# Optimization experiments

Measured on AMD Instinct MI355X. Metric: run time of the kernel, lower is better.

The kernel has to match this reference:

```python
import jax, jax.numpy as jnp
import numpy as np

DIM = 512
HEADS = 8
WIN = 64


def setup_inputs() -> dict:
    key = jax.random.key(0)
    k1, k2, k3 = jax.random.split(key, 3)
    x = jax.random.normal(k1, (16, 4096, DIM), dtype=jnp.float32)
    Wqkv = jax.random.normal(k2, (DIM, 3 * DIM), dtype=jnp.float32) * 0.02
    Wproj = jax.random.normal(k3, (DIM, DIM), dtype=jnp.float32) * 0.02
    bproj = jnp.zeros((DIM,), dtype=jnp.float32)
    return {"x": x, "Wqkv": Wqkv, "Wproj": Wproj, "bproj": bproj}


def reference(x, Wqkv, Wproj, bproj):
    B0, T0, C = x.shape
    H = HEADS
    hd = C // H
    scale = hd ** -0.5
    # reshape sequence into fixed-size windows: [Bw, W, C]
    xw = x.reshape(-1, WIN, C)
    Bw = xw.shape[0]
    # fused QKV projection (no bias)
    qkv = (xw @ Wqkv).reshape(Bw, WIN, 3, H, hd)
    qkv = jnp.transpose(qkv, (2, 0, 3, 1, 4))  # [3, Bw, H, W, hd]
    q, k, v = qkv[0], qkv[1], qkv[2]
    attn = jnp.einsum('bhqd,bhkd->bhqk', q, k) * scale  # [Bw, H, W, W]
    # causal mask within each window
    mask = jnp.tril(jnp.ones((WIN, WIN), dtype=bool))
    attn = jnp.where(mask, attn, -jnp.inf)
    attn = jax.nn.softmax(attn, axis=-1)
    # faithful to source: second (unconditional) softmax applied on probabilities
    attn = jax.nn.softmax(attn, axis=-1)
    out = jnp.einsum('bhqk,bhkd->bhqd', attn, v)  # [Bw, H, W, hd]
    out = jnp.transpose(out, (0, 2, 1, 3)).reshape(Bw, WIN, C)
    out = out @ Wproj + bproj
    return out.reshape(B0, T0, C)
```

## Files before the change

### kernel.cpp

```cpp
#include <hip/hip_runtime.h>


typedef _Float16 f16x8 __attribute__((ext_vector_type(8)));
typedef _Float16 f16x4 __attribute__((ext_vector_type(4)));
typedef float f32x4 __attribute__((ext_vector_type(4)));

#define MFMA16(a, b, c) __builtin_amdgcn_mfma_f32_16x16x32_f16((a), (b), (c), 0, 0, 0)

__device__ __forceinline__ int swz64(int r, int c) { return r * 64 + (c ^ ((r & 7) << 3)); }
__device__ __forceinline__ int swz512(int r, int c) { return r * 512 + (c ^ ((r & 7) << 3)); }

typedef const __attribute__((address_space(1))) void* gas1_t;
typedef __attribute__((address_space(3))) void* las3_t;

__device__ __forceinline__ void stage16(const _Float16* g, _Float16* lbase, int lane) {
#if __has_builtin(__builtin_amdgcn_global_load_lds)
  __builtin_amdgcn_global_load_lds((gas1_t)(const void*)g, (las3_t)(void*)lbase, 16, 0, 0);
#else
  *(f16x8*)(lbase + lane * 8) = *(const f16x8*)g;
#endif
}

__global__ void prep_weights(const float* __restrict__ Wqkv,
                             const float* __restrict__ Wproj,
                             _Float16* __restrict__ wqkvP,
                             _Float16* __restrict__ wprojP) {
  int idx = blockIdx.x * blockDim.x + threadIdx.x;
  if (idx < 786432) {
    int r16 = idx >> 13;
    int rem = idx & 8191;
    int kt = rem >> 9;
    int lane = (rem >> 3) & 63;
    int e = rem & 7;
    int row = r16 * 16 + (lane & 15);
    int k = kt * 32 + (lane >> 4) * 8 + e;
    float v = Wqkv[k * 1536 + row];
    if (row < 512) v *= 0.125f;
    wqkvP[idx] = (_Float16)v;
  } else {
    int j = idx - 786432;
    int r16 = j >> 13;
    int rem = j & 8191;
    int kt = rem >> 9;
    int lane = (rem >> 3) & 63;
    int e = rem & 7;
    int n = r16 * 16 + (lane & 15);
    int k = kt * 32 + (lane >> 4) * 8 + e;
    wprojP[j] = (_Float16)Wproj[k * 512 + n];
  }
}

__global__ __launch_bounds__(512) void prep_x(const float* __restrict__ x,
                                              _Float16* __restrict__ xP) {
  __shared__ __align__(16) _Float16 sX[64 * 512];
  const int tid = threadIdx.x;
  const float4* xv = (const float4*)(x + (size_t)blockIdx.x * 32768);
#pragma unroll
  for (int it = 0; it < 8; ++it) {
    int g = tid + it * 512;
    int r = g >> 6, c0 = (g & 63) << 3;
    float4 a = xv[(r << 7) + (c0 >> 2)];
    float4 b = xv[(r << 7) + (c0 >> 2) + 1];
    f16x8 hv;
    hv[0] = (_Float16)a.x; hv[1] = (_Float16)a.y;
    hv[2] = (_Float16)a.z; hv[3] = (_Float16)a.w;
    hv[4] = (_Float16)b.x; hv[5] = (_Float16)b.y;
    hv[6] = (_Float16)b.z; hv[7] = (_Float16)b.w;
    *(f16x8*)&sX[swz512(r, c0)] = hv;
  }
  __syncthreads();
  _Float16* dst = xP + (size_t)blockIdx.x * 32768;
#pragma unroll
  for (int it = 0; it < 8; ++it) {
    int c8 = tid + it * 512;
    int rt = c8 >> 10, ks = (c8 >> 6) & 15, ln = c8 & 63;
    int row = rt * 16 + (ln & 15);
    int k0 = ks * 32 + (ln >> 4) * 8;
    f16x8 v = *(const f16x8*)&sX[swz512(row, k0)];
    *(f16x8*)(dst + c8 * 8) = v;
  }
}

template <int MODE>
__global__ __launch_bounds__(1024, 4) void gemmT(
    const _Float16* __restrict__ Afp, const _Float16* __restrict__ Bfp,
    _Float16* __restrict__ dst16, float* __restrict__ out,
    const float* __restrict__ bproj) {
  __shared__ __align__(16) _Float16 sG[2][2][16][512];
  const int tid = threadIdx.x;
  const int wid = tid >> 6;
  const int lane = tid & 63;
  const int lg = lane >> 4, lr = lane & 15;
  const int wr = wid >> 2, wc = wid & 3;
  const int r0 = blockIdx.x * 256, c0 = blockIdx.y * 256;

  const _Float16* aS = Afp + (size_t)((r0 >> 4) + wid) * 8192 + lane * 8;
  const _Float16* bS = Bfp + (size_t)((c0 >> 4) + wid) * 8192 + lane * 8;

  const f32x4 zero4 = {0.f, 0.f, 0.f, 0.f};
  f32x4 acc[4][4];
#pragma unroll
  for (int i = 0; i < 4; ++i)
#pragma unroll
    for (int j = 0; j < 4; ++j) acc[i][j] = zero4;

  stage16(aS, &sG[0][0][wid][0], lane);
  stage16(bS, &sG[0][1][wid][0], lane);
  __syncthreads();

  for (int kt = 0; kt < 16; ++kt) {
    const int cur = kt & 1;
    if (kt < 15) {
      stage16(aS + (kt + 1) * 512, &sG[cur ^ 1][0][wid][0], lane);
      stage16(bS + (kt + 1) * 512, &sG[cur ^ 1][1][wid][0], lane);
    }
    f16x8 af[4], bf[4];
#pragma unroll
    for (int mi = 0; mi < 4; ++mi)
      af[mi] = *(const f16x8*)&sG[cur][0][wr * 4 + mi][lane * 8];
#pragma unroll
    for (int ni = 0; ni < 4; ++ni)
      bf[ni] = *(const f16x8*)&sG[cur][1][wc * 4 + ni][lane * 8];
#pragma unroll
    for (int mi = 0; mi < 4; ++mi)
#pragma unroll
      for (int ni = 0; ni < 4; ++ni)
        acc[mi][ni] = MFMA16(af[mi], bf[ni], acc[mi][ni]);
    __syncthreads();
  }

  if constexpr (MODE == 0) {
#pragma unroll
    for (int mi = 0; mi < 4; ++mi) {
      int nb = r0 + wr * 64 + mi * 16 + lg * 4;
      int sec = nb >> 9, h = (nb >> 6) & 7, db = nb & 63;
      int e0 = db & 7;
      int coff = (db >> 5) * 512 + (((db >> 3) & 3) * 16) * 8 + e0;
#pragma unroll
      for (int ni = 0; ni < 4; ++ni) {
        int tg = c0 + wc * 64 + ni * 16 + lr;
        int w = tg >> 6, t = tg & 63;
        size_t pos = ((size_t)w * 24 + sec * 8 + h) * 4096 +
                     (size_t)((t >> 4) * 2) * 512 + coff + (t & 15) * 8;
        f16x4 hv;
        hv[0] = (_Float16)acc[mi][ni][0]; hv[1] = (_Float16)acc[mi][ni][1];
        hv[2] = (_Float16)acc[mi][ni][2]; hv[3] = (_Float16)acc[mi][ni][3];
        *(f16x4*)(dst16 + pos) = hv;
      }
    }
  } else if constexpr (MODE == 1) {
#pragma unroll
    for (int mi = 0; mi < 4; ++mi) {
      int tbg = r0 + wr * 64 + mi * 16 + lg * 4;
      int w = tbg >> 6, tb = tbg & 63;
      int e0 = tb & 7;
      int coff = (tb >> 5) * 512 + (((tb >> 3) & 3) * 16) * 8 + e0;
#pragma unroll
      for (int ni = 0; ni < 4; ++ni) {
        int cv = c0 + wc * 64 + ni * 16 + lr;
        int h = cv >> 6, d = cv & 63;
        size_t pos = ((size_t)w * 24 + 16 + h) * 4096 +
                     (size_t)((d >> 4) * 2) * 512 + coff + (d & 15) * 8;
        f16x4 hv;
        hv[0] = (_Float16)acc[mi][ni][0]; hv[1] = (_Float16)acc[mi][ni][1];
        hv[2] = (_Float16)acc[mi][ni][2]; hv[3] = (_Float16)acc[mi][ni][3];
        *(f16x4*)(dst16 + pos) = hv;
      }
    }
  } else {
#pragma unroll
    for (int mi = 0; mi < 4; ++mi) {
      int nb = r0 + wr * 64 + mi * 16 + lg * 4;
      float4 bi = *(const float4*)&bproj[nb];
#pragma unroll
      for (int ni = 0; ni < 4; ++ni) {
        int tg = c0 + wc * 64 + ni * 16 + lr;
        float4 v;
        v.x = acc[mi][ni][0] + bi.x; v.y = acc[mi][ni][1] + bi.y;
        v.z = acc[mi][ni][2] + bi.z; v.w = acc[mi][ni][3] + bi.w;
        *(float4*)&out[(size_t)tg * 512 + nb] = v;
      }
    }
  }
}

__global__ __launch_bounds__(512, 4) void attn_win(
    const _Float16* __restrict__ qkvP, _Float16* __restrict__ hP) {
  __shared__ __align__(16) _Float16 sP[4][4096];
  const int tid = threadIdx.x;
  const int wid = tid >> 6;
  const int lane = tid & 63;
  const int lg = lane >> 4, lr = lane & 15;
  const int hl = wid >> 1, part = wid & 1;
  const int w = blockIdx.x;
  const f32x4 zero4 = {0.f, 0.f, 0.f, 0.f};

  for (int hr = 0; hr < 2; ++hr) {
    const int h = hr * 4 + hl;
    const _Float16* Qb = qkvP + ((size_t)w * 24 + h) * 4096 + lane * 8;
    const _Float16* Kb = qkvP + ((size_t)w * 24 + 8 + h) * 4096 + lane * 8;
    const _Float16* Vb = qkvP + ((size_t)w * 24 + 16 + h) * 4096 + lane * 8;

    f16x8 afq[2][2], bfk[4][2];
#pragma unroll
    for (int rs = 0; rs < 2; ++rs)
#pragma unroll
      for (int dkt = 0; dkt < 2; ++dkt)
        afq[rs][dkt] = *(const f16x8*)(Qb + ((part * 2 + rs) * 2 + dkt) * 512);
#pragma unroll
    for (int nt = 0; nt < 4; ++nt)
#pragma unroll
      for (int dkt = 0; dkt < 2; ++dkt)
        bfk[nt][dkt] = *(const f16x8*)(Kb + (nt * 2 + dkt) * 512);
    f32x4 sacc[2][4];
#pragma unroll
    for (int rs = 0; rs < 2; ++rs)
#pragma unroll
      for (int nt = 0; nt < 4; ++nt) sacc[rs][nt] = zero4;
#pragma unroll
    for (int dkt = 0; dkt < 2; ++dkt)
#pragma unroll
      for (int rs = 0; rs < 2; ++rs)
#pragma unroll
        for (int nt = 0; nt < 4; ++nt)
          sacc[rs][nt] = MFMA16(afq[rs][dkt], bfk[nt][dkt], sacc[rs][nt]);

    f16x8 afv[2][2];
#pragma unroll
    for (int ds = 0; ds < 2; ++ds)
#pragma unroll
      for (int tkt = 0; tkt < 2; ++tkt)
        afv[ds][tkt] = *(const f16x8*)(Vb + ((part * 2 + ds) * 2 + tkt) * 512);

    float p2[2][4][4];
#pragma unroll
    for (int rs = 0; rs < 2; ++rs) {
      const int rsg = part * 2 + rs;
#pragma unroll
      for (int rg = 0; rg < 4; ++rg) {
        int row = rsg * 16 + lg * 4 + rg;
        float m = -1e30f;
#pragma unroll
        for (int nt = 0; nt < 4; ++nt) {
          int col = nt * 16 + lr;
          float v = (col <= row) ? sacc[rs][nt][rg] : -1e30f;
          m = fmaxf(m, v);
        }
#pragma unroll
        for (int off = 8; off >= 1; off >>= 1) m = fmaxf(m, __shfl_xor(m, off));
        float e[4], s1 = 0.f;
#pragma unroll
        for (int nt = 0; nt < 4; ++nt) {
          int col = nt * 16 + lr;
          e[nt] = (col <= row) ? __expf(sacc[rs][nt][rg] - m) : 0.f;
          s1 += e[nt];
        }
#pragma unroll
        for (int off = 8; off >= 1; off >>= 1) s1 += __shfl_xor(s1, off);
        float inv1 = 1.f / s1;
        float e2[4], s2 = 0.f;
#pragma unroll
        for (int nt = 0; nt < 4; ++nt) {
          e2[nt] = __expf(e[nt] * inv1);
          s2 += e2[nt];
        }
#pragma unroll
        for (int off = 8; off >= 1; off >>= 1) s2 += __shfl_xor(s2, off);
        float inv2 = 1.f / s2;
#pragma unroll
        for (int nt = 0; nt < 4; ++nt) p2[rs][nt][rg] = e2[nt] * inv2;
      }
    }

#pragma unroll
    for (int rs = 0; rs < 2; ++rs) {
      const int rsg = part * 2 + rs;
#pragma unroll
      for (int nt = 0; nt < 4; ++nt) {
        int cbase = (rsg * 2 + (nt >> 1)) * 512 +
                    ((((nt * 2) + (lr >> 3)) & 3) * 16 + lg * 4) * 8 + (lr & 7);
#pragma unroll
        for (int rg = 0; rg < 4; ++rg)
          sP[hl][cbase + rg * 8] = (_Float16)p2[rs][nt][rg];
      }
    }
    __syncthreads();

    f32x4 oacc[2][4];
#pragma unroll
    for (int ds = 0; ds < 2; ++ds)
#pragma unroll
      for (int ntq = 0; ntq < 4; ++ntq) oacc[ds][ntq] = zero4;
#pragma unroll
    for (int tkt = 0; tkt < 2; ++tkt) {
      f16x8 bfp[4];
#pragma unroll
      for (int ntq = 0; ntq < 4; ++ntq)
        bfp[ntq] = *(const f16x8*)&sP[hl][(ntq * 2 + tkt) * 512 + lane * 8];
#pragma unroll
      for (int ds = 0; ds < 2; ++ds)
#pragma unroll
        for (int ntq = 0; ntq < 4; ++ntq)
          oacc[ds][ntq] = MFMA16(afv[ds][tkt], bfp[ntq], oacc[ds][ntq]);
    }

#pragma unroll
    for (int ds = 0; ds < 2; ++ds) {
      const int dsg = part * 2 + ds;
      const int e0 = (lg & 1) * 4;
      const int lgt = (dsg * 2 + (lg >> 1)) & 3;
#pragma unroll
      for (int ntq = 0; ntq < 4; ++ntq) {
        size_t pos = ((size_t)(w * 4 + ntq) * 16 + h * 2 + (dsg >> 1)) * 512 +
                     (lgt * 16 + lr) * 8 + e0;
        f16x4 hv;
        hv[0] = (_Float16)oacc[ds][ntq][0]; hv[1] = (_Float16)oacc[ds][ntq][1];
        hv[2] = (_Float16)oacc[ds][ntq][2]; hv[3] = (_Float16)oacc[ds][ntq][3];
        *(f16x4*)(hP + pos) = hv;
      }
    }
    __syncthreads();
  }
}

__global__ __launch_bounds__(512, 2) void attn_fused(
    const float* __restrict__ x, const _Float16* __restrict__ wqkvP,
    const _Float16* __restrict__ wprojP, const float* __restrict__ bproj,
    float* __restrict__ out) {
  __shared__ __align__(16) _Float16 sX[64 * 512];
  __shared__ __align__(16) _Float16 sHeads[4][2][4096];

  const int tid = threadIdx.x;
  const int wid = tid >> 6;
  const int lane = tid & 63;
  const int lg = lane >> 4;
  const int lr = lane & 15;

  _Float16* sQ0 = &sHeads[0][0][0];
  _Float16* sK0 = &sHeads[1][0][0];
  _Float16* sVT0 = &sHeads[2][0][0];
  _Float16* sPO0 = &sHeads[3][0][0];

  const float4* xv = (const float4*)(x + (size_t)blockIdx.x * 32768);
#pragma unroll
  for (int it = 0; it < 8; ++it) {
    int g = tid + it * 512;
    int r = g >> 6, c0 = (g & 63) << 3;
    float4 a = xv[(r << 7) + (c0 >> 2)];
    float4 b = xv[(r << 7) + (c0 >> 2) + 1];
    f16x8 hv;
    hv[0] = (_Float16)a.x; hv[1] = (_Float16)a.y;
    hv[2] = (_Float16)a.z; hv[3] = (_Float16)a.w;
    hv[4] = (_Float16)b.x; hv[5] = (_Float16)b.y;
    hv[6] = (_Float16)b.z; hv[7] = (_Float16)b.w;
    *(f16x8*)&sX[swz512(r, c0)] = hv;
  }
  const f32x4 zero4 = {0.f, 0.f, 0.f, 0.f};
  f32x4 accO[4][4];
#pragma unroll
  for (int i = 0; i < 4; ++i)
#pragma unroll
    for (int j = 0; j < 4; ++j) accO[i][j] = zero4;
  __syncthreads();

  for (int hp = 0; hp < 4; ++hp) {
    int hu[3], su[3], stu[3];
    const _Float16* bp[3];
    f32x4 acc[3][4];
#pragma unroll
    for (int i = 0; i < 3; ++i) {
      int u = wid + 8 * i;
      int hh = u & 1, v2 = u >> 1;
      int sec = v2 % 3, strip = v2 / 3;
      hu[i] = hh; su[i] = sec; stu[i] = strip;
      int r16 = sec * 32 + (hp * 2 + hh) * 4 + strip;
      bp[i] = wqkvP + (size_t)r16 * 8192 + lane * 8;
#pragma unroll
      for (int rt = 0; rt < 4; ++rt) acc[i][rt] = zero4;
    }
    f16x8 bf[3][3];
#pragma unroll
    for (int d = 0; d < 3; ++d)
#pragma unroll
      for (int i = 0; i < 3; ++i) bf[d][i] = *(const f16x8*)(bp[i] + d * 512);
    f16x8 af[2][4];
#pragma unroll
    for (int rt = 0; rt < 4; ++rt)
      af[0][rt] = *(const f16x8*)&sX[swz512(rt * 16 + lr, lg * 8)];
#pragma unroll
    for (int ks = 0; ks < 16; ++ks) {
      if (ks < 15) {
#pragma unroll
        for (int rt = 0; rt < 4; ++rt)
          af[(ks + 1) & 1][rt] =
              *(const f16x8*)&sX[swz512(rt * 16 + lr, (ks + 1) * 32 + lg * 8)];
      }
#pragma unroll
      for (int i = 0; i < 3; ++i)
#pragma unroll
        for (int rt = 0; rt < 4; ++rt)
          acc[i][rt] = MFMA16(af[ks & 1][rt], bf[ks % 3][i], acc[i][rt]);
      if (ks + 3 < 16) {
#pragma unroll
        for (int i = 0; i < 3; ++i)
          bf[ks % 3][i] = *(const f16x8*)(bp[i] + (ks + 3) * 512);
      }
    }
#pragma unroll
    for (int i = 0; i < 3; ++i) {
      int hh = hu[i], sec = su[i], strip = stu[i];
      _Float16* dq = sQ0 + hh * 4096;
      _Float16* dk = sK0 + hh * 4096;
      _Float16* dv = sVT0 + hh * 4096;
#pragma unroll
      for (int rt = 0; rt < 4; ++rt)
#pragma unroll
        for (int rg = 0; rg < 4; ++rg) {
          int row = rt * 16 + lg * 4 + rg;
          int col = strip * 16 + lr;
          _Float16 v = (_Float16)acc[i][rt][rg];
          if (sec == 0) dq[swz64(row, col)] = v;
          else if (sec == 1) dk[swz64(row, col)] = v;
          else dv[swz64(col, row)] = v;
        }
    }
    __syncthreads();
    {
      const int hh = wid >> 2;
      const int rs = wid & 3;
      const _Float16* mQ = sQ0 + hh * 4096;
      const _Float16* mK = sK0 + hh * 4096;
      const _Float16* mV = sVT0 + hh * 4096;
      _Float16* mP = sPO0 + hh * 4096;
      f32x4 sacc[4];
#pragma unroll
      for (int nt = 0; nt < 4; ++nt) sacc[nt] = zero4;
#pragma unroll
      for (int ks = 0; ks < 2; ++ks) {
        f16x8 afq = *(const f16x8*)&mQ[swz64(rs * 16 + lr, ks * 32 + lg * 8)];
#pragma unroll
        for (int nt = 0; nt < 4; ++nt) {
          f16x8 bfk = *(const f16x8*)&mK[swz64(nt * 16 + lr, ks * 32 + lg * 8)];
          sacc[nt] = MFMA16(afq, bfk, sacc[nt]);
        }
      }
      float p2[4][4];
#pragma unroll
      for (int rg = 0; rg < 4; ++rg) {
        int row = rs * 16 + lg * 4 + rg;
        float m = -1e30f;
#pragma unroll
        for (int nt = 0; nt < 4; ++nt) {
          int col = nt * 16 + lr;
          float v = (col <= row) ? sacc[nt][rg] : -1e30f;
          m = fmaxf(m, v);
        }
#pragma unroll
        for (int off = 8; off >= 1; off >>= 1) m = fmaxf(m, __shfl_xor(m, off));
        float e[4], s1 = 0.f;
#pragma unroll
        for (int nt = 0; nt < 4; ++nt) {
          int col = nt * 16 + lr;
          e[nt] = (col <= row) ? __expf(sacc[nt][rg] - m) : 0.f;
          s1 += e[nt];
        }
#pragma unroll
        for (int off = 8; off >= 1; off >>= 1) s1 += __shfl_xor(s1, off);
        float inv1 = 1.f / s1;
        float e2[4], s2 = 0.f;
#pragma unroll
        for (int nt = 0; nt < 4; ++nt) {
          e2[nt] = __expf(e[nt] * inv1);
          s2 += e2[nt];
        }
#pragma unroll
        for (int off = 8; off >= 1; off >>= 1) s2 += __shfl_xor(s2, off);
        float inv2 = 1.f / s2;
#pragma unroll
        for (int nt = 0; nt < 4; ++nt) p2[nt][rg] = e2[nt] * inv2;
      }
#pragma unroll
      for (int nt = 0; nt < 4; ++nt)
#pragma unroll
        for (int rg = 0; rg < 4; ++rg)
          mP[swz64(rs * 16 + lg * 4 + rg, nt * 16 + lr)] = (_Float16)p2[nt][rg];
      asm volatile("" ::: "memory");
      f32x4 oacc[4];
#pragma unroll
      for (int nt = 0; nt < 4; ++nt) oacc[nt] = zero4;
#pragma unroll
      for (int ks = 0; ks < 2; ++ks) {
        f16x8 afp = *(const f16x8*)&mP[swz64(rs * 16 + lr, ks * 32 + lg * 8)];
#pragma unroll
        for (int nt = 0; nt < 4; ++nt) {
          f16x8 bfv = *(const f16x8*)&mV[swz64(nt * 16 + lr, ks * 32 + lg * 8)];
          oacc[nt] = MFMA16(afp, bfv, oacc[nt]);
        }
      }
      asm volatile("" ::: "memory");
#pragma unroll
      for (int nt = 0; nt < 4; ++nt)
#pragma unroll
        for (int rg = 0; rg < 4; ++rg)
          mP[swz64(rs * 16 + lg * 4 + rg, nt * 16 + lr)] = (_Float16)oacc[nt][rg];
    }
    __syncthreads();
    {
      f16x8 bfC[2][4], afC[2][4];
#pragma unroll
      for (int rt = 0; rt < 4; ++rt)
        afC[0][rt] = *(const f16x8*)&sPO0[swz64(rt * 16 + lr, lg * 8)];
#pragma unroll
      for (int nt = 0; nt < 4; ++nt)
        bfC[0][nt] = *(const f16x8*)(wprojP + (size_t)(wid * 4 + nt) * 8192 +
                                     (size_t)(hp * 4) * 512 + lane * 8);
#pragma unroll
      for (int g = 0; g < 4; ++g) {
        if (g < 3) {
          int hn = (g + 1) >> 1, kn = (g + 1) & 1;
#pragma unroll
          for (int rt = 0; rt < 4; ++rt)
            afC[(g + 1) & 1][rt] = *(const f16x8*)&sPO0[hn * 4096 +
                swz64(rt * 16 + lr, kn * 32 + lg * 8)];
#pragma unroll
          for (int nt = 0; nt < 4; ++nt)
            bfC[(g + 1) & 1][nt] =
                *(const f16x8*)(wprojP + (size_t)(wid * 4 + nt) * 8192 +
                                (size_t)(hp * 4 + g + 1) * 512 + lane * 8);
        }
#pragma unroll
        for (int nt = 0; nt < 4; ++nt)
#pragma unroll
          for (int rt = 0; rt < 4; ++rt)
            accO[rt][nt] = MFMA16(afC[g & 1][rt], bfC[g & 1][nt], accO[rt][nt]);
      }
    }
  }
  __syncthreads();
  float bias_r[4];
#pragma unroll
  for (int nt = 0; nt < 4; ++nt) bias_r[nt] = bproj[wid * 64 + nt * 16 + lr];
  float* sEp = (float*)&sHeads[0][0][0];
  size_t base = (size_t)blockIdx.x * 32768;
#pragma unroll
  for (int half = 0; half < 2; ++half) {
#pragma unroll
    for (int rr = 0; rr < 2; ++rr) {
      int rt = half * 2 + rr;
#pragma unroll
      for (int nt = 0; nt < 4; ++nt)
#pragma unroll
        for (int rg = 0; rg < 4; ++rg) {
          int r = rr * 16 + lg * 4 + rg;
          int c = wid * 64 + nt * 16 + lr;
          sEp[r * 512 + (c ^ (((r >> 2) & 1) << 4))] = accO[rt][nt][rg] + bias_r[nt];
        }
    }
    __syncthreads();
#pragma unroll
    for (int j = 0; j < 8; ++j) {
      int f4 = tid + j * 512;
      int r = f4 >> 7;
      int c0 = (f4 & 127) << 2;
      float4 v = *(const float4*)&sEp[r * 512 + (c0 ^ (((r >> 2) & 1) << 4))];
      *(float4*)&out[base + (size_t)(half * 32 + r) * 512 + c0] = v;
    }
    if (half == 0) __syncthreads();
  }
}

extern "C" void kernel_launch(void* const* d_in, const int* in_sizes, int n_in,
                              void* d_out, int out_size, void* d_ws, size_t ws_size,
                              hipStream_t stream) {
  const float* x = (const float*)d_in[0];
  const float* Wqkv = (const float*)d_in[1];
  const float* Wproj = (const float*)d_in[2];
  const float* bproj = (const float*)d_in[3];
  float* out = (float*)d_out;

  const size_t W1 = 786432, W2 = 262144, XN = 33554432;
  const size_t QN = 100663296, HN = 33554432;
  _Float16* wqkvP = (_Float16*)d_ws;
  _Float16* wprojP = wqkvP + W1;
  _Float16* xP = wprojP + W2;
  _Float16* qkvP = xP + XN;
  _Float16* hP = qkvP + QN;
  const size_t NEED = (W1 + W2 + XN + QN + HN) * 2;

  prep_weights<<<dim3(4096), dim3(256), 0, stream>>>(Wqkv, Wproj, wqkvP, wprojP);
  if (ws_size >= NEED) {
    prep_x<<<dim3(1024), dim3(512), 0, stream>>>(x, xP);
    gemmT<0><<<dim3(4, 256), dim3(1024), 0, stream>>>(wqkvP, xP, qkvP, nullptr, nullptr);
    gemmT<1><<<dim3(256, 2), dim3(1024), 0, stream>>>(xP, wqkvP + (size_t)64 * 8192,
                                                      qkvP, nullptr, nullptr);
    attn_win<<<dim3(1024), dim3(512), 0, stream>>>(qkvP, hP);
    gemmT<2><<<dim3(2, 256), dim3(1024), 0, stream>>>(wprojP, hP, nullptr, out, bproj);
  } else {
    attn_fused<<<dim3(1024), dim3(512), 0, stream>>>(x, wqkvP, wprojP, bproj, out);
  }
}
```

Baseline: 312.8 us.

## Replace GEMM kernels with 8-wave ping-pong pipelined GEMM and XCD-aware tile swizzle

Replaces the 16-wave 256x256 GEMM with an 8-wave version in which each wave computes a 128x64 sub-tile. K is processed in 64-wide steps, and loading the next stage is interleaved with four quarter-MFMA phases separated by raw s_barrier and explicit vmcnt waits. MFMA sections run at raised s_setprio. The block index is remapped round-robin across 8 groups so neighbouring tiles share L2. The intent is to hide global-to-LDS latency behind MFMA work and raise MFMA density per wave, at the cost of more registers (launch bounds 512,2), many barriers, and hand-written waitcnt logic that is fragile to get right.

```diff
diff --git a/kernel.cpp b/kernel.cpp
--- a/kernel.cpp
+++ b/kernel.cpp
@@ -20,6 +20,9 @@
   *(f16x8*)(lbase + lane * 8) = *(const f16x8*)g;
 #endif
 }
+
+#define CFENCE() asm volatile("" ::: "memory")
+#define BARRIER() do { CFENCE(); __builtin_amdgcn_s_barrier(); CFENCE(); } while (0)
 
 __global__ void prep_weights(const float* __restrict__ Wqkv,
                              const float* __restrict__ Wproj,
@@ -81,61 +84,141 @@
   }
 }
 
+__device__ __forceinline__ void ds_a4(const _Float16* base, int chunkBase, int lane8,
+                                      f16x8 (&a)[4][2]) {
+#pragma unroll
+  for (int mi = 0; mi < 4; ++mi)
+#pragma unroll
+    for (int kt = 0; kt < 2; ++kt)
+      a[mi][kt] = *(const f16x8*)(base + (chunkBase + mi * 2 + kt) * 512 + lane8);
+}
+
+__device__ __forceinline__ void ds_b2(const _Float16* base, int chunkBase, int lane8,
+                                      f16x8 (&b)[2][2]) {
+#pragma unroll
+  for (int ni = 0; ni < 2; ++ni)
+#pragma unroll
+    for (int kt = 0; kt < 2; ++kt)
+      b[ni][kt] = *(const f16x8*)(base + (chunkBase + ni * 2 + kt) * 512 + lane8);
+}
+
+__device__ __forceinline__ void mma_q(const f16x8 (&a)[4][2], const f16x8 (&b)[2][2],
+                                      f32x4 (&acc)[8][4], int rh, int ch) {
+  __builtin_amdgcn_s_setprio(1);
+#pragma unroll
+  for (int kt = 0; kt < 2; ++kt)
+#pragma unroll
+    for (int mi = 0; mi < 4; ++mi)
+#pragma unroll
+      for (int ni = 0; ni < 2; ++ni)
+        acc[rh * 4 + mi][ch * 2 + ni] =
+            MFMA16(a[mi][kt], b[ni][kt], acc[rh * 4 + mi][ch * 2 + ni]);
+  __builtin_amdgcn_s_setprio(0);
+}
+
 template <int MODE>
-__global__ __launch_bounds__(1024, 4) void gemmT(
+__global__ __launch_bounds__(512, 2) void gemm8(
     const _Float16* __restrict__ Afp, const _Float16* __restrict__ Bfp,
     _Float16* __restrict__ dst16, float* __restrict__ out,
-    const float* __restrict__ bproj) {
-  __shared__ __align__(16) _Float16 sG[2][2][16][512];
+    const float* __restrict__ bproj, int rTiles) {
+  __shared__ __align__(16) _Float16 sG[2][2][32][512];
   const int tid = threadIdx.x;
   const int wid = tid >> 6;
   const int lane = tid & 63;
   const int lg = lane >> 4, lr = lane & 15;
   const int wr = wid >> 2, wc = wid & 3;
-  const int r0 = blockIdx.x * 256, c0 = blockIdx.y * 256;
-
-  const _Float16* aS = Afp + (size_t)((r0 >> 4) + wid) * 8192 + lane * 8;
-  const _Float16* bS = Bfp + (size_t)((c0 >> 4) + wid) * 8192 + lane * 8;
+  const int wr8 = wr * 8, wc4 = wc * 4, lane8 = lane * 8;
+
+  const int nwg = gridDim.x;
+  const int bid = blockIdx.x;
+  const int swz = (bid & 7) * (nwg >> 3) + (bid >> 3);
+  const int r0 = (swz % rTiles) * 256, c0 = (swz / rTiles) * 256;
+
+  const _Float16* Abase = Afp + (size_t)(r0 >> 4) * 8192 + lane8;
+  const _Float16* Bbase = Bfp + (size_t)(c0 >> 4) * 8192 + lane8;
+  const _Float16* sA0 = &sG[0][0][0][0];
+  const _Float16* sB0 = &sG[0][1][0][0];
+  const _Float16* sA1 = &sG[1][0][0][0];
+  const _Float16* sB1 = &sG[1][1][0][0];
+
+  auto STAGE = [&](int s, int h, int T) {
+    const int r16 = ((h & 1) << 3) + wid;
+    if (h < 2) {
+      const _Float16* src = Abase + (size_t)r16 * 8192 + (size_t)T * 1024;
+      stage16(src, &sG[s][0][r16 * 2][0], lane);
+      stage16(src + 512, &sG[s][0][r16 * 2 + 1][0], lane);
+    } else {
+      const _Float16* src = Bbase + (size_t)r16 * 8192 + (size_t)T * 1024;
+      stage16(src, &sG[s][1][r16 * 2][0], lane);
+      stage16(src + 512, &sG[s][1][r16 * 2 + 1][0], lane);
+    }
+  };
 
   const f32x4 zero4 = {0.f, 0.f, 0.f, 0.f};
-  f32x4 acc[4][4];
-#pragma unroll
-  for (int i = 0; i < 4; ++i)
+  f32x4 acc[8][4];
+#pragma unroll
+  for (int i = 0; i < 8; ++i)
 #pragma unroll
     for (int j = 0; j < 4; ++j) acc[i][j] = zero4;
 
-  stage16(aS, &sG[0][0][wid][0], lane);
-  stage16(bS, &sG[0][1][wid][0], lane);
-  __syncthreads();
-
-  for (int kt = 0; kt < 16; ++kt) {
-    const int cur = kt & 1;
-    if (kt < 15) {
-      stage16(aS + (kt + 1) * 512, &sG[cur ^ 1][0][wid][0], lane);
-      stage16(bS + (kt + 1) * 512, &sG[cur ^ 1][1][wid][0], lane);
-    }
-    f16x8 af[4], bf[4];
-#pragma unroll
-    for (int mi = 0; mi < 4; ++mi)
-      af[mi] = *(const f16x8*)&sG[cur][0][wr * 4 + mi][lane * 8];
-#pragma unroll
-    for (int ni = 0; ni < 4; ++ni)
-      bf[ni] = *(const f16x8*)&sG[cur][1][wc * 4 + ni][lane * 8];
-#pragma unroll
-    for (int mi = 0; mi < 4; ++mi)
-#pragma unroll
-      for (int ni = 0; ni < 4; ++ni)
-        acc[mi][ni] = MFMA16(af[mi], bf[ni], acc[mi][ni]);
-    __syncthreads();
+  f16x8 a[4][2], b0[2][2], b1[2][2];
+
+#pragma unroll
+  for (int h = 0; h < 4; ++h) STAGE(0, h, 0);
+
+  for (int i = 0; i < 4; ++i) {
+    const int T1 = 2 * i + 1;
+    const int T2 = (2 * i + 2 > 7) ? 7 : 2 * i + 2;
+    STAGE(1, 0, T1);
+    asm volatile("s_waitcnt vmcnt(2)" ::: "memory");
+    BARRIER();
+    ds_a4(sA0, wr8 * 2, lane8, a);
+    ds_b2(sB0, wc4 * 2, lane8, b0);
+    mma_q(a, b0, acc, 0, 0);
+    BARRIER();
+    ds_b2(sB0, (wc4 + 2) * 2, lane8, b1);
+    STAGE(1, 1, T1);
+    BARRIER();
+    mma_q(a, b1, acc, 0, 1);
+    BARRIER();
+    ds_a4(sA0, (wr8 + 4) * 2, lane8, a);
+    STAGE(1, 2, T1);
+    BARRIER();
+    mma_q(a, b1, acc, 1, 1);
+    BARRIER();
+    STAGE(1, 3, T1);
+    BARRIER();
+    mma_q(a, b0, acc, 1, 0);
+    BARRIER();
+    STAGE(0, 0, T2);
+    asm volatile("s_waitcnt vmcnt(2)" ::: "memory");
+    BARRIER();
+    ds_a4(sA1, wr8 * 2, lane8, a);
+    ds_b2(sB1, wc4 * 2, lane8, b0);
+    mma_q(a, b0, acc, 0, 0);
+    BARRIER();
+    ds_b2(sB1, (wc4 + 2) * 2, lane8, b1);
+    STAGE(0, 1, T2);
+    BARRIER();
+    mma_q(a, b1, acc, 0, 1);
+    BARRIER();
+    ds_a4(sA1, (wr8 + 4) * 2, lane8, a);
+    STAGE(0, 2, T2);
+    BARRIER();
+    mma_q(a, b1, acc, 1, 1);
+    BARRIER();
+    STAGE(0, 3, T2);
+    BARRIER();
+    mma_q(a, b0, acc, 1, 0);
+    BARRIER();
   }
 
   if constexpr (MODE == 0) {
 #pragma unroll
-    for (int mi = 0; mi < 4; ++mi) {
-      int nb = r0 + wr * 64 + mi * 16 + lg * 4;
+    for (int mi = 0; mi < 8; ++mi) {
+      int nb = r0 + wr * 128 + mi * 16 + lg * 4;
       int sec = nb >> 9, h = (nb >> 6) & 7, db = nb & 63;
-      int e0 = db & 7;
-      int coff = (db >> 5) * 512 + (((db >> 3) & 3) * 16) * 8 + e0;
+      int coff = (db >> 5) * 512 + (((db >> 3) & 3) * 16) * 8 + (db & 7);
 #pragma unroll
       for (int ni = 0; ni < 4; ++ni) {
         int tg = c0 + wc * 64 + ni * 16 + lr;
@@ -150,11 +233,10 @@
     }
   } else if constexpr (MODE == 1) {
 #pragma unroll
-    for (int mi = 0; mi < 4; ++mi) {
-      int tbg = r0 + wr * 64 + mi * 16 + lg * 4;
+    for (int mi = 0; mi < 8; ++mi) {
+      int tbg = r0 + wr * 128 + mi * 16 + lg * 4;
       int w = tbg >> 6, tb = tbg & 63;
-      int e0 = tb & 7;
-      int coff = (tb >> 5) * 512 + (((tb >> 3) & 3) * 16) * 8 + e0;
+      int coff = (tb >> 5) * 512 + (((tb >> 3) & 3) * 16) * 8 + (tb & 7);
 #pragma unroll
       for (int ni = 0; ni < 4; ++ni) {
         int cv = c0 + wc * 64 + ni * 16 + lr;
@@ -169,8 +251,8 @@
     }
   } else {
 #pragma unroll
-    for (int mi = 0; mi < 4; ++mi) {
-      int nb = r0 + wr * 64 + mi * 16 + lg * 4;
+    for (int mi = 0; mi < 8; ++mi) {
+      int nb = r0 + wr * 128 + mi * 16 + lg * 4;
       float4 bi = *(const float4*)&bproj[nb];
 #pragma unroll
       for (int ni = 0; ni < 4; ++ni) {
@@ -590,11 +672,11 @@
   prep_weights<<<dim3(4096), dim3(256), 0, stream>>>(Wqkv, Wproj, wqkvP, wprojP);
   if (ws_size >= NEED) {
     prep_x<<<dim3(1024), dim3(512), 0, stream>>>(x, xP);
-    gemmT<0><<<dim3(4, 256), dim3(1024), 0, stream>>>(wqkvP, xP, qkvP, nullptr, nullptr);
-    gemmT<1><<<dim3(256, 2), dim3(1024), 0, stream>>>(xP, wqkvP + (size_t)64 * 8192,
-                                                      qkvP, nullptr, nullptr);
+    gemm8<0><<<dim3(1024), dim3(512), 0, stream>>>(wqkvP, xP, qkvP, nullptr, nullptr, 4);
+    gemm8<1><<<dim3(512), dim3(512), 0, stream>>>(xP, wqkvP + (size_t)64 * 8192,
+                                                  qkvP, nullptr, nullptr, 256);
     attn_win<<<dim3(1024), dim3(512), 0, stream>>>(qkvP, hP);
-    gemmT<2><<<dim3(2, 256), dim3(1024), 0, stream>>>(wprojP, hP, nullptr, out, bproj);
+    gemm8<2><<<dim3(512), dim3(512), 0, stream>>>(wprojP, hP, nullptr, out, bproj, 2);
   } else {
     attn_fused<<<dim3(1024), dim3(512), 0, stream>>>(x, wqkvP, wprojP, bproj, out);
   }
```

After: 295.5 us. 5.5% less time.
